# Kernel tuning notes

Measured on AMD Instinct MI355X. Metric: run time of the kernel, lower is better.

## Reference

```python
import jax, jax.numpy as jnp
import numpy as np

B, IN_DIM, HID, N_WIRES = 8192, 2048, 2048, 8


def setup_inputs() -> dict:
    key = jax.random.key(0)
    ks = jax.random.split(key, 12)
    fan_in = IN_DIM + HID
    w_scale = 1.0 / np.sqrt(fan_in)  # ~ nn.Linear default init scale
    mk_w = lambda k: jax.random.normal(k, (N_WIRES, fan_in), jnp.float32) * w_scale
    mk_b = lambda k: jax.random.normal(k, (N_WIRES,), jnp.float32) * w_scale
    return {
        "x": jax.random.normal(ks[0], (B, IN_DIM), jnp.float32),
        "hx": jax.random.normal(ks[1], (B, HID), jnp.float32),
        "cx": jax.random.normal(ks[2], (B, HID), jnp.float32),
        "Wf": mk_w(ks[3]), "bf": mk_b(ks[4]),
        "Wi": mk_w(ks[5]), "bi": mk_b(ks[6]),
        "Wg": mk_w(ks[7]), "bg": mk_b(ks[8]),
        "Wo": mk_w(ks[9]), "bo": mk_b(ks[10]),
    }


def reference(x, hx, cx, Wf, bf, Wi, bi, Wg, bg, Wo, bo):
    combined = jnp.concatenate([x, hx], axis=1)  # [B, IN+HID]
    # Exact expectation of the RX-only circuit: E[#zeros - #ones] = sum_i cos(angle_i)
    q_exp = lambda W, b: jnp.sum(jnp.cos(combined @ W.T + b))
    f = jax.nn.sigmoid(q_exp(Wf, bf))
    i = jax.nn.sigmoid(q_exp(Wi, bi))
    g = jnp.tanh(q_exp(Wg, bg))
    o = jax.nn.sigmoid(q_exp(Wo, bo))
    cx_new = f * cx + i * g
    hx_new = o * jnp.tanh(cx_new)
    return hx_new, cx_new
```

## Files before the change

### kernel.cpp

```cpp
#include <hip/hip_runtime.h>
#include <hip/hip_bf16.h>
#include <cstdint>
#include <cstddef>

#define B_ROWS 8192
#define KDIM   4096
#define IN_DIM 2048
#define HIDDEN 2048
#define NJ     32
#define KC     8
#define CHUNK  (KDIM / KC)
#define BK     64
#define SUBT   (CHUNK / BK)
#define MROWS  64
#define NBUF   4

typedef __bf16 bf16x8 __attribute__((ext_vector_type(8)));
typedef __bf16 bf16x4 __attribute__((ext_vector_type(4)));
typedef float  f32x4  __attribute__((ext_vector_type(4)));

__device__ __forceinline__ bf16x8 cvt8(f32x4 a, f32x4 b) {
    bf16x8 r;
    r[0] = (__bf16)a.x; r[1] = (__bf16)a.y; r[2] = (__bf16)a.z; r[3] = (__bf16)a.w;
    r[4] = (__bf16)b.x; r[5] = (__bf16)b.y; r[6] = (__bf16)b.z; r[7] = (__bf16)b.w;
    return r;
}

__device__ __forceinline__ void gload_lds16(const void* g, void* lds) {
    __builtin_amdgcn_global_load_lds(
        (const __attribute__((address_space(1))) void*)g,
        (__attribute__((address_space(3))) void*)lds, 16, 0, 0);
}

extern "C" __global__ __launch_bounds__(256)
void w_pack(const float* __restrict__ Wf, const float* __restrict__ Wi,
            const float* __restrict__ Wg, const float* __restrict__ Wo,
            __bf16* __restrict__ Wb, float* __restrict__ q)
{
    if (blockIdx.x == 0 && threadIdx.x < 4) q[threadIdx.x] = 0.f;

    const int t    = blockIdx.x * 256 + threadIdx.x;
    const int idx4 = t << 2;
    const int j    = idx4 >> 12;
    const int k    = idx4 & (KDIM - 1);
    const float* W = (j < 8) ? Wf : (j < 16) ? Wi : (j < 24) ? Wg : Wo;
    f32x4 v = *reinterpret_cast<const f32x4*>(W + (size_t)(j & 7) * KDIM + k);
    bf16x4 b;
    b[0] = (__bf16)v.x; b[1] = (__bf16)v.y; b[2] = (__bf16)v.z; b[3] = (__bf16)v.w;
    *reinterpret_cast<bf16x4*>(Wb + idx4) = b;
}

extern "C" __global__ __launch_bounds__(256)
void p1_mfma(const float* __restrict__ x, const float* __restrict__ hx,
             const __bf16* __restrict__ Wb, float* __restrict__ Spart)
{
    __shared__ float  Abuf[NBUF][MROWS * BK];
    __shared__ __bf16 Bbuf[NBUF][NJ * BK];

    const int bid  = blockIdx.x;
    const int kc   = bid & (KC - 1);
    const int mb   = bid >> 3;
    const int tid  = threadIdx.x;
    const int wave = tid >> 6;
    const int lane = tid & 63;
    const int rowblk = mb * MROWS;
    const int k0   = kc * CHUNK;

    const float* Aglob = (kc < 4)
        ? (x  + (size_t)rowblk * IN_DIM + k0)
        : (hx + (size_t)rowblk * HIDDEN + (k0 - IN_DIM));
    const __bf16* Bglob = Wb + k0;

    int aOff[4];
#pragma unroll
    for (int p = 0; p < 4; ++p) {
        const int r  = wave * 16 + p * 4 + (lane >> 4);
        const int cs = (lane & 15) ^ ((p * 4 + (lane >> 4)) & 7);
        aOff[p] = r * 2048 + cs * 4;
    }
    const int bj   = wave * 8 + (lane >> 3);
    const int bOff = bj * KDIM + (((lane & 7) ^ ((lane >> 3) & 7)) * 8);

    const int lrow  = lane & 15;
    const int row_r = wave * 16 + lrow;
    int offA0[2], offA1[2], offB0[2], offB1[2];
#pragma unroll
    for (int st = 0; st < 2; ++st) {
        const int cu = st * 8 + (lane >> 4) * 2;
        offA0[st] = row_r * 256 + ((cu + 0) ^ (lane & 7)) * 16;
        offA1[st] = row_r * 256 + ((cu + 1) ^ (lane & 7)) * 16;
        const int cb = st * 4 + (lane >> 4);
        offB0[st] = lrow * 128        + (cb ^ (lrow & 7)) * 16;
        offB1[st] = (lrow + 16) * 128 + (cb ^ (lrow & 7)) * 16;
    }

    f32x4 acc0 = {0.f, 0.f, 0.f, 0.f};
    f32x4 acc1 = {0.f, 0.f, 0.f, 0.f};

    auto issue = [&](int s) {
        const int b = s & (NBUF - 1);
#pragma unroll
        for (int p = 0; p < 4; ++p)
            gload_lds16(Aglob + aOff[p] + s * BK, &Abuf[b][(wave * 4 + p) * 256]);
        gload_lds16(Bglob + bOff + s * BK, &Bbuf[b][wave * 512]);
    };
    auto compute = [&](int s) {
        const int b = s & (NBUF - 1);
        const char* Ab = (const char*)&Abuf[b][0];
        const char* Bb = (const char*)&Bbuf[b][0];
#pragma unroll
        for (int st = 0; st < 2; ++st) {
            f32x4 a0 = *reinterpret_cast<const f32x4*>(Ab + offA0[st]);
            f32x4 a1 = *reinterpret_cast<const f32x4*>(Ab + offA1[st]);
            bf16x8 af = cvt8(a0, a1);
            bf16x8 b0 = *reinterpret_cast<const bf16x8*>(Bb + offB0[st]);
            bf16x8 b1 = *reinterpret_cast<const bf16x8*>(Bb + offB1[st]);
            acc0 = __builtin_amdgcn_mfma_f32_16x16x32_bf16(af, b0, acc0, 0, 0, 0);
            acc1 = __builtin_amdgcn_mfma_f32_16x16x32_bf16(af, b1, acc1, 0, 0, 0);
        }
    };

    issue(0);
    issue(1);
#pragma unroll
    for (int s = 0; s < SUBT; ++s) {
        if (s + 2 < SUBT) issue(s + 2);
        if (s < SUBT - 2)
            asm volatile("s_waitcnt vmcnt(10)" ::: "memory");
        else if (s == SUBT - 2)
            asm volatile("s_waitcnt vmcnt(5)" ::: "memory");
        else
            asm volatile("s_waitcnt vmcnt(0)" ::: "memory");
        __builtin_amdgcn_s_barrier();
        __builtin_amdgcn_sched_barrier(0);
        compute(s);
    }

    const int row0 = rowblk + wave * 16;
    float* sp = Spart + ((size_t)kc * B_ROWS + row0) * NJ;
    const int m0 = (lane >> 4) * 4;
#pragma unroll
    for (int r = 0; r < 4; ++r) {
        sp[(size_t)(m0 + r) * NJ + lrow]      = acc0[r];
        sp[(size_t)(m0 + r) * NJ + 16 + lrow] = acc1[r];
    }
}

extern "C" __global__ __launch_bounds__(256)
void p2_cos_reduce(const float* __restrict__ Spart,
                   const float* __restrict__ bf, const float* __restrict__ bi,
                   const float* __restrict__ bg, const float* __restrict__ bo,
                   float* __restrict__ q)
{
    __shared__ float ql[4];
    if (threadIdx.x < 4) ql[threadIdx.x] = 0.f;
    __syncthreads();

    const int t    = blockIdx.x * 256 + threadIdx.x;
    const int j    = t & 31;
    const int gate = j >> 3;
    const float* Bp = (gate == 0) ? bf : (gate == 1) ? bi : (gate == 2) ? bg : bo;
    const float bj = Bp[j & 7];

    float accg = 0.f;
#pragma unroll
    for (int i = 0; i < 4; ++i) {
        const int row = (t >> 5) + i * 2048;
        float s = 0.f;
#pragma unroll
        for (int kc = 0; kc < KC; ++kc)
            s += Spart[((size_t)kc * B_ROWS + row) * NJ + j];
        accg += cosf(s + bj);
    }

    accg += __shfl_xor(accg, 1, 64);
    accg += __shfl_xor(accg, 2, 64);
    accg += __shfl_xor(accg, 4, 64);
    if ((threadIdx.x & 7) == 0) atomicAdd(&ql[gate], accg);
    __syncthreads();
    if (threadIdx.x < 4) atomicAdd(&q[threadIdx.x], ql[threadIdx.x]);
}

extern "C" __global__ __launch_bounds__(256)
void p3_elementwise(const float* __restrict__ cx, const float* __restrict__ q,
                    float* __restrict__ out)
{
    const float qf = q[0], qi = q[1], qg = q[2], qo = q[3];
    const float f  = 1.f / (1.f + expf(-qf));
    const float ii = 1.f / (1.f + expf(-qi));
    const float g  = tanhf(qg);
    const float o  = 1.f / (1.f + expf(-qo));
    const float ig = ii * g;

    const size_t N  = (size_t)B_ROWS * HIDDEN;
    const size_t N4 = N >> 2;
    const f32x4* cx4 = (const f32x4*)cx;
    f32x4* outh = (f32x4*)out;
    f32x4* outc = (f32x4*)(out + N);

    for (size_t idx = (size_t)blockIdx.x * blockDim.x + threadIdx.x; idx < N4;
         idx += (size_t)gridDim.x * blockDim.x) {
        f32x4 c = __builtin_nontemporal_load(cx4 + idx);
        f32x4 cn, hn;
        cn.x = fmaf(f, c.x, ig);
        cn.y = fmaf(f, c.y, ig);
        cn.z = fmaf(f, c.z, ig);
        cn.w = fmaf(f, c.w, ig);
        hn.x = o * tanhf(cn.x);
        hn.y = o * tanhf(cn.y);
        hn.z = o * tanhf(cn.z);
        hn.w = o * tanhf(cn.w);
        outc[idx] = cn;
        outh[idx] = hn;
    }
}

extern "C" void kernel_launch(void* const* d_in, const int* in_sizes, int n_in,
                              void* d_out, int out_size, void* d_ws, size_t ws_size,
                              hipStream_t stream)
{
    const float* x  = (const float*)d_in[0];
    const float* hx = (const float*)d_in[1];
    const float* cx = (const float*)d_in[2];
    const float* Wf = (const float*)d_in[3];
    const float* bf = (const float*)d_in[4];
    const float* Wi = (const float*)d_in[5];
    const float* bi = (const float*)d_in[6];
    const float* Wg = (const float*)d_in[7];
    const float* bg = (const float*)d_in[8];
    const float* Wo = (const float*)d_in[9];
    const float* bo = (const float*)d_in[10];
    float* out = (float*)d_out;

    float*   Spart = (float*)d_ws;
    __bf16*  Wb    = (__bf16*)(Spart + (size_t)KC * B_ROWS * NJ);
    float*   q     = (float*)(Wb + (size_t)NJ * KDIM);

    w_pack<<<dim3(128), dim3(256), 0, stream>>>(Wf, Wi, Wg, Wo, Wb, q);
    p1_mfma<<<dim3(128 * KC), dim3(256), 0, stream>>>(x, hx, Wb, Spart);
    p2_cos_reduce<<<dim3(256), dim3(256), 0, stream>>>(Spart, bf, bi, bg, bo, q);
    p3_elementwise<<<dim3(2048), dim3(256), 0, stream>>>(cx, q, out);
}
```

Baseline: 76.30 us.

## Fuse all four stages into one cooperative persistent kernel with grid syncs

Replaces the four separate launches (weight pack, MFMA GEMM, cos-reduce, elementwise) with one cooperative kernel of 256 blocks. The stages are separated by grid.sync, and each block loops over four GEMM tiles. The aim is to remove launch overhead and inter-kernel gaps. In exchange, occupancy drops to 256 single-block-per-CU workgroups, which may reduce latency hiding in the GEMM and the memory-bound elementwise phase, and three grid-wide barriers are added.

```diff
diff --git a/kernel.cpp b/kernel.cpp
--- a/kernel.cpp
+++ b/kernel.cpp
@@ -1,7 +1,10 @@
 #include <hip/hip_runtime.h>
+#include <hip/hip_cooperative_groups.h>
 #include <hip/hip_bf16.h>
 #include <cstdint>
 #include <cstddef>
+
+namespace cg = cooperative_groups;
 
 #define B_ROWS 8192
 #define KDIM   4096
@@ -14,6 +17,9 @@
 #define SUBT   (CHUNK / BK)
 #define MROWS  64
 #define NBUF   4
+#define NTILE  1024
+#define GRID   256
+#define TIERS  (NTILE / GRID)
 
 typedef __bf16 bf16x8 __attribute__((ext_vector_type(8)));
 typedef __bf16 bf16x4 __attribute__((ext_vector_type(4)));
@@ -32,44 +38,44 @@
         (__attribute__((address_space(3))) void*)lds, 16, 0, 0);
 }
 
-extern "C" __global__ __launch_bounds__(256)
-void w_pack(const float* __restrict__ Wf, const float* __restrict__ Wi,
-            const float* __restrict__ Wg, const float* __restrict__ Wo,
-            __bf16* __restrict__ Wb, float* __restrict__ q)
-{
-    if (blockIdx.x == 0 && threadIdx.x < 4) q[threadIdx.x] = 0.f;
-
-    const int t    = blockIdx.x * 256 + threadIdx.x;
-    const int idx4 = t << 2;
-    const int j    = idx4 >> 12;
-    const int k    = idx4 & (KDIM - 1);
-    const float* W = (j < 8) ? Wf : (j < 16) ? Wi : (j < 24) ? Wg : Wo;
-    f32x4 v = *reinterpret_cast<const f32x4*>(W + (size_t)(j & 7) * KDIM + k);
-    bf16x4 b;
-    b[0] = (__bf16)v.x; b[1] = (__bf16)v.y; b[2] = (__bf16)v.z; b[3] = (__bf16)v.w;
-    *reinterpret_cast<bf16x4*>(Wb + idx4) = b;
-}
-
-extern "C" __global__ __launch_bounds__(256)
-void p1_mfma(const float* __restrict__ x, const float* __restrict__ hx,
-             const __bf16* __restrict__ Wb, float* __restrict__ Spart)
+extern "C" __global__ __launch_bounds__(256, 1)
+void fused_all(const float* __restrict__ x,  const float* __restrict__ hx,
+               const float* __restrict__ cx,
+               const float* __restrict__ Wf, const float* __restrict__ bfp,
+               const float* __restrict__ Wi, const float* __restrict__ bip,
+               const float* __restrict__ Wg, const float* __restrict__ bgp,
+               const float* __restrict__ Wo, const float* __restrict__ bop,
+               float* __restrict__ out, float* __restrict__ Spart,
+               __bf16* __restrict__ Wb, float* __restrict__ q)
 {
     __shared__ float  Abuf[NBUF][MROWS * BK];
     __shared__ __bf16 Bbuf[NBUF][NJ * BK];
-
-    const int bid  = blockIdx.x;
-    const int kc   = bid & (KC - 1);
-    const int mb   = bid >> 3;
-    const int tid  = threadIdx.x;
+    __shared__ float  ql[4];
+
+    cg::grid_group grid = cg::this_grid();
+    const int bid = blockIdx.x;
+    const int tid = threadIdx.x;
+
+    {
+        const int t = bid * 256 + tid;
+        if (t < (NJ * KDIM / 4)) {
+            const int idx4 = t << 2;
+            const int j    = idx4 >> 12;
+            const int k    = idx4 & (KDIM - 1);
+            const float* W = (j < 8) ? Wf : (j < 16) ? Wi : (j < 24) ? Wg : Wo;
+            f32x4 v = *reinterpret_cast<const f32x4*>(W + (size_t)(j & 7) * KDIM + k);
+            bf16x4 b;
+            b[0] = (__bf16)v.x; b[1] = (__bf16)v.y;
+            b[2] = (__bf16)v.z; b[3] = (__bf16)v.w;
+            *reinterpret_cast<bf16x4*>(Wb + idx4) = b;
+        }
+        if (bid == 0 && tid < 4) q[tid] = 0.f;
+    }
+    grid.sync();
+
     const int wave = tid >> 6;
     const int lane = tid & 63;
-    const int rowblk = mb * MROWS;
-    const int k0   = kc * CHUNK;
-
-    const float* Aglob = (kc < 4)
-        ? (x  + (size_t)rowblk * IN_DIM + k0)
-        : (hx + (size_t)rowblk * HIDDEN + (k0 - IN_DIM));
-    const __bf16* Bglob = Wb + k0;
+    const int lrow = lane & 15;
 
     int aOff[4];
 #pragma unroll
@@ -81,7 +87,6 @@
     const int bj   = wave * 8 + (lane >> 3);
     const int bOff = bj * KDIM + (((lane & 7) ^ ((lane >> 3) & 7)) * 8);
 
-    const int lrow  = lane & 15;
     const int row_r = wave * 16 + lrow;
     int offA0[2], offA1[2], offB0[2], offB1[2];
 #pragma unroll
@@ -94,124 +99,132 @@
         offB1[st] = (lrow + 16) * 128 + (cb ^ (lrow & 7)) * 16;
     }
 
-    f32x4 acc0 = {0.f, 0.f, 0.f, 0.f};
-    f32x4 acc1 = {0.f, 0.f, 0.f, 0.f};
-
-    auto issue = [&](int s) {
-        const int b = s & (NBUF - 1);
-#pragma unroll
-        for (int p = 0; p < 4; ++p)
-            gload_lds16(Aglob + aOff[p] + s * BK, &Abuf[b][(wave * 4 + p) * 256]);
-        gload_lds16(Bglob + bOff + s * BK, &Bbuf[b][wave * 512]);
-    };
-    auto compute = [&](int s) {
-        const int b = s & (NBUF - 1);
-        const char* Ab = (const char*)&Abuf[b][0];
-        const char* Bb = (const char*)&Bbuf[b][0];
-#pragma unroll
-        for (int st = 0; st < 2; ++st) {
-            f32x4 a0 = *reinterpret_cast<const f32x4*>(Ab + offA0[st]);
-            f32x4 a1 = *reinterpret_cast<const f32x4*>(Ab + offA1[st]);
-            bf16x8 af = cvt8(a0, a1);
-            bf16x8 b0 = *reinterpret_cast<const bf16x8*>(Bb + offB0[st]);
-            bf16x8 b1 = *reinterpret_cast<const bf16x8*>(Bb + offB1[st]);
-            acc0 = __builtin_amdgcn_mfma_f32_16x16x32_bf16(af, b0, acc0, 0, 0, 0);
-            acc1 = __builtin_amdgcn_mfma_f32_16x16x32_bf16(af, b1, acc1, 0, 0, 0);
-        }
-    };
-
-    issue(0);
-    issue(1);
-#pragma unroll
-    for (int s = 0; s < SUBT; ++s) {
-        if (s + 2 < SUBT) issue(s + 2);
-        if (s < SUBT - 2)
-            asm volatile("s_waitcnt vmcnt(10)" ::: "memory");
-        else if (s == SUBT - 2)
-            asm volatile("s_waitcnt vmcnt(5)" ::: "memory");
-        else
-            asm volatile("s_waitcnt vmcnt(0)" ::: "memory");
-        __builtin_amdgcn_s_barrier();
-        __builtin_amdgcn_sched_barrier(0);
-        compute(s);
-    }
-
-    const int row0 = rowblk + wave * 16;
-    float* sp = Spart + ((size_t)kc * B_ROWS + row0) * NJ;
-    const int m0 = (lane >> 4) * 4;
-#pragma unroll
-    for (int r = 0; r < 4; ++r) {
-        sp[(size_t)(m0 + r) * NJ + lrow]      = acc0[r];
-        sp[(size_t)(m0 + r) * NJ + 16 + lrow] = acc1[r];
-    }
-}
-
-extern "C" __global__ __launch_bounds__(256)
-void p2_cos_reduce(const float* __restrict__ Spart,
-                   const float* __restrict__ bf, const float* __restrict__ bi,
-                   const float* __restrict__ bg, const float* __restrict__ bo,
-                   float* __restrict__ q)
-{
-    __shared__ float ql[4];
-    if (threadIdx.x < 4) ql[threadIdx.x] = 0.f;
-    __syncthreads();
-
-    const int t    = blockIdx.x * 256 + threadIdx.x;
-    const int j    = t & 31;
-    const int gate = j >> 3;
-    const float* Bp = (gate == 0) ? bf : (gate == 1) ? bi : (gate == 2) ? bg : bo;
-    const float bj = Bp[j & 7];
-
-    float accg = 0.f;
-#pragma unroll
-    for (int i = 0; i < 4; ++i) {
-        const int row = (t >> 5) + i * 2048;
-        float s = 0.f;
-#pragma unroll
-        for (int kc = 0; kc < KC; ++kc)
-            s += Spart[((size_t)kc * B_ROWS + row) * NJ + j];
-        accg += cosf(s + bj);
-    }
-
-    accg += __shfl_xor(accg, 1, 64);
-    accg += __shfl_xor(accg, 2, 64);
-    accg += __shfl_xor(accg, 4, 64);
-    if ((threadIdx.x & 7) == 0) atomicAdd(&ql[gate], accg);
-    __syncthreads();
-    if (threadIdx.x < 4) atomicAdd(&q[threadIdx.x], ql[threadIdx.x]);
-}
-
-extern "C" __global__ __launch_bounds__(256)
-void p3_elementwise(const float* __restrict__ cx, const float* __restrict__ q,
-                    float* __restrict__ out)
-{
-    const float qf = q[0], qi = q[1], qg = q[2], qo = q[3];
-    const float f  = 1.f / (1.f + expf(-qf));
-    const float ii = 1.f / (1.f + expf(-qi));
-    const float g  = tanhf(qg);
-    const float o  = 1.f / (1.f + expf(-qo));
-    const float ig = ii * g;
-
-    const size_t N  = (size_t)B_ROWS * HIDDEN;
-    const size_t N4 = N >> 2;
-    const f32x4* cx4 = (const f32x4*)cx;
-    f32x4* outh = (f32x4*)out;
-    f32x4* outc = (f32x4*)(out + N);
-
-    for (size_t idx = (size_t)blockIdx.x * blockDim.x + threadIdx.x; idx < N4;
-         idx += (size_t)gridDim.x * blockDim.x) {
-        f32x4 c = __builtin_nontemporal_load(cx4 + idx);
-        f32x4 cn, hn;
-        cn.x = fmaf(f, c.x, ig);
-        cn.y = fmaf(f, c.y, ig);
-        cn.z = fmaf(f, c.z, ig);
-        cn.w = fmaf(f, c.w, ig);
-        hn.x = o * tanhf(cn.x);
-        hn.y = o * tanhf(cn.y);
-        hn.z = o * tanhf(cn.z);
-        hn.w = o * tanhf(cn.w);
-        outc[idx] = cn;
-        outh[idx] = hn;
+#pragma unroll 1
+    for (int tier = 0; tier < TIERS; ++tier) {
+        const int tile = bid + tier * GRID;
+        const int kc   = tile & (KC - 1);
+        const int mb   = tile >> 3;
+        const int rowblk = mb * MROWS;
+        const int k0   = kc * CHUNK;
+
+        const float* Aglob = (kc < 4)
+            ? (x  + (size_t)rowblk * IN_DIM + k0)
+            : (hx + (size_t)rowblk * HIDDEN + (k0 - IN_DIM));
+        const __bf16* Bglob = Wb + k0;
+
+        f32x4 acc0 = {0.f, 0.f, 0.f, 0.f};
+        f32x4 acc1 = {0.f, 0.f, 0.f, 0.f};
+
+        auto issue = [&](int s) {
+            const int b = s & (NBUF - 1);
+#pragma unroll
+            for (int p = 0; p < 4; ++p)
+                gload_lds16(Aglob + aOff[p] + s * BK, &Abuf[b][(wave * 4 + p) * 256]);
+            gload_lds16(Bglob + bOff + s * BK, &Bbuf[b][wave * 512]);
+        };
+        auto compute = [&](int s) {
+            const int b = s & (NBUF - 1);
+            const char* Ab = (const char*)&Abuf[b][0];
+            const char* Bb = (const char*)&Bbuf[b][0];
+#pragma unroll
+            for (int st = 0; st < 2; ++st) {
+                f32x4 a0 = *reinterpret_cast<const f32x4*>(Ab + offA0[st]);
+                f32x4 a1 = *reinterpret_cast<const f32x4*>(Ab + offA1[st]);
+                bf16x8 af = cvt8(a0, a1);
+                bf16x8 b0 = *reinterpret_cast<const bf16x8*>(Bb + offB0[st]);
+                bf16x8 b1 = *reinterpret_cast<const bf16x8*>(Bb + offB1[st]);
+                acc0 = __builtin_amdgcn_mfma_f32_16x16x32_bf16(af, b0, acc0, 0, 0, 0);
+                acc1 = __builtin_amdgcn_mfma_f32_16x16x32_bf16(af, b1, acc1, 0, 0, 0);
+            }
+        };
+
+        issue(0);
+        issue(1);
+#pragma unroll
+        for (int s = 0; s < SUBT; ++s) {
+            if (s + 2 < SUBT) issue(s + 2);
+            if (s < SUBT - 2)
+                asm volatile("s_waitcnt vmcnt(10)" ::: "memory");
+            else if (s == SUBT - 2)
+                asm volatile("s_waitcnt vmcnt(5)" ::: "memory");
+            else
+                asm volatile("s_waitcnt vmcnt(0)" ::: "memory");
+            __builtin_amdgcn_s_barrier();
+            __builtin_amdgcn_sched_barrier(0);
+            compute(s);
+        }
+
+        const int row0 = rowblk + wave * 16;
+        float* sp = Spart + ((size_t)kc * B_ROWS + row0) * NJ;
+        const int m0 = (lane >> 4) * 4;
+#pragma unroll
+        for (int r = 0; r < 4; ++r) {
+            sp[(size_t)(m0 + r) * NJ + lrow]      = acc0[r];
+            sp[(size_t)(m0 + r) * NJ + 16 + lrow] = acc1[r];
+        }
+    }
+    grid.sync();
+
+    {
+        if (tid < 4) ql[tid] = 0.f;
+        __syncthreads();
+
+        const int gt   = bid * 256 + tid;
+        const int j    = gt & 31;
+        const int gate = j >> 3;
+        const float* Bp = (gate == 0) ? bfp : (gate == 1) ? bip
+                        : (gate == 2) ? bgp : bop;
+        const float bjv = Bp[j & 7];
+
+        float accg = 0.f;
+#pragma unroll
+        for (int i = 0; i < 4; ++i) {
+            const int row = (gt >> 5) + i * 2048;
+            float s = 0.f;
+#pragma unroll
+            for (int kc = 0; kc < KC; ++kc)
+                s += Spart[((size_t)kc * B_ROWS + row) * NJ + j];
+            accg += cosf(s + bjv);
+        }
+        accg += __shfl_xor(accg, 1, 64);
+        accg += __shfl_xor(accg, 2, 64);
+        accg += __shfl_xor(accg, 4, 64);
+        if ((tid & 7) == 0) atomicAdd(&ql[gate], accg);
+        __syncthreads();
+        if (tid < 4) atomicAdd(&q[tid], ql[tid]);
+    }
+    grid.sync();
+
+    {
+        const float qf = q[0], qi = q[1], qg = q[2], qo = q[3];
+        const float f  = 1.f / (1.f + expf(-qf));
+        const float ii = 1.f / (1.f + expf(-qi));
+        const float g  = tanhf(qg);
+        const float o  = 1.f / (1.f + expf(-qo));
+        const float ig = ii * g;
+
+        const size_t N  = (size_t)B_ROWS * HIDDEN;
+        const int    gt = bid * 256 + tid;
+        const f32x4* cx4 = (const f32x4*)cx;
+        f32x4* outh = (f32x4*)out;
+        f32x4* outc = (f32x4*)(out + N);
+
+#pragma unroll 4
+        for (int it = 0; it < 64; ++it) {
+            const size_t idx = (size_t)it * 65536 + gt;
+            f32x4 c = __builtin_nontemporal_load(cx4 + idx);
+            f32x4 cn, hn;
+            cn.x = fmaf(f, c.x, ig);
+            cn.y = fmaf(f, c.y, ig);
+            cn.z = fmaf(f, c.z, ig);
+            cn.w = fmaf(f, c.w, ig);
+            hn.x = o * tanhf(cn.x);
+            hn.y = o * tanhf(cn.y);
+            hn.z = o * tanhf(cn.z);
+            hn.w = o * tanhf(cn.w);
+            outc[idx] = cn;
+            outh[idx] = hn;
+        }
     }
 }
 
@@ -236,8 +249,12 @@
     __bf16*  Wb    = (__bf16*)(Spart + (size_t)KC * B_ROWS * NJ);
     float*   q     = (float*)(Wb + (size_t)NJ * KDIM);
 
-    w_pack<<<dim3(128), dim3(256), 0, stream>>>(Wf, Wi, Wg, Wo, Wb, q);
-    p1_mfma<<<dim3(128 * KC), dim3(256), 0, stream>>>(x, hx, Wb, Spart);
-    p2_cos_reduce<<<dim3(256), dim3(256), 0, stream>>>(Spart, bf, bi, bg, bo, q);
-    p3_elementwise<<<dim3(2048), dim3(256), 0, stream>>>(cx, q, out);
-}
+    void* args[] = {
+        (void*)&x,  (void*)&hx, (void*)&cx,
+        (void*)&Wf, (void*)&bf, (void*)&Wi, (void*)&bi,
+        (void*)&Wg, (void*)&bg, (void*)&Wo, (void*)&bo,
+        (void*)&out, (void*)&Spart, (void*)&Wb, (void*)&q
+    };
+    hipLaunchCooperativeKernel(reinterpret_cast<void*>(fused_all),
+                               dim3(GRID), dim3(256), args, 0, stream);
+}
```

Result: slower. 183.6 us (+140.6%).
